# Optimization experiments

Measured on AMD Instinct MI355X. Metric: run time of the kernel, lower is better.

## Reference

```python
import jax, jax.numpy as jnp
import numpy as np

D_MODEL = 512
NUM_HEADS = 8
D_HEAD = D_MODEL // NUM_HEADS
QMAX = 127.0  # int8 narrow-range symmetric
EPS = 1e-8


def _quant_dequant_weight(w):
    # per-output-channel symmetric int8 quant-dequant (brevitas default style)
    s = jnp.maximum(jnp.max(jnp.abs(w), axis=1, keepdims=True) / QMAX, EPS)
    return jnp.clip(jnp.round(w / s), -QMAX, QMAX) * s


def _quant_dequant_act(x):
    # per-tensor symmetric int8 quant-dequant (QuantIdentity)
    s = jnp.maximum(jnp.max(jnp.abs(x)) / QMAX, EPS)
    return jnp.clip(jnp.round(x / s), -QMAX, QMAX) * s


def _qlinear(x, w, b):
    return jnp.einsum('btd,od->bto', x, _quant_dequant_weight(w)) + b


def setup_inputs() -> dict:
    key = jax.random.key(0)
    ks = jax.random.split(key, 10)
    B, T = 2, 4096
    lim = 1.0 / np.sqrt(D_MODEL)
    mk = lambda k: jax.random.uniform(k, (D_MODEL, D_MODEL), jnp.float32, -lim, lim)
    mb = lambda k: jax.random.uniform(k, (D_MODEL,), jnp.float32, -lim, lim)
    return {
        'x': jax.random.normal(ks[0], (B, T, D_MODEL), jnp.float32),
        'mask': jax.random.randint(ks[1], (B, T), 0, 2, jnp.int32),
        'Wq': mk(ks[2]), 'bq': mb(ks[3]),
        'Wk': mk(ks[4]), 'bk': mb(ks[5]),
        'Wv': mk(ks[6]), 'bv': mb(ks[7]),
        'Wo': mk(ks[8]), 'bo': mb(ks[9]),
    }


def reference(x, mask, Wq, bq, Wk, bk, Wv, bv, Wo, bo):
    B, T, _ = x.shape
    shape = lambda t: t.reshape(B, T, NUM_HEADS, D_HEAD).transpose(0, 2, 1, 3)  # (B,H,T,dh)
    q = shape(_qlinear(x, Wq, bq))
    k = shape(_qlinear(x, Wk, bk))
    v = shape(_qlinear(x, Wv, bv))
    scores = jnp.einsum('bhtd,bhsd->bhts', q, k) / np.sqrt(D_HEAD)
    keep = (mask != 0)[:, None, None, :]  # (B,1,1,T), 0 = masked
    scores = jnp.where(keep, scores, -jnp.inf)
    attn = jax.nn.softmax(scores, axis=-1)
    ctx = jnp.einsum('bhts,bhsd->bhtd', attn, v)
    ctx = ctx.transpose(0, 2, 1, 3).reshape(B, T, D_MODEL)
    out = _qlinear(ctx, Wo, bo)
    return _quant_dequant_act(out)
```

## Files before the change

### kernel.cpp

```cpp
#include <hip/hip_runtime.h>
#include <hip/hip_bf16.h>

typedef __bf16 bf16;
typedef __bf16 bf16x8 __attribute__((ext_vector_type(8)));
typedef __bf16 bf16x4v __attribute__((ext_vector_type(4)));
typedef float f32x4 __attribute__((ext_vector_type(4)));

#define D_MODEL 512
#define T_SEQ   4096
#define NH      8
#define DH      64
#define M_ROWS  8192
#define VROW    8224
#define QK_SCALE 0.18033688011112042f

__device__ __forceinline__ void gload16(const void* g, void* l) {
  __builtin_amdgcn_global_load_lds(
      (const __attribute__((address_space(1))) unsigned int*)g,
      (__attribute__((address_space(3))) unsigned int*)l, 16, 0, 0);
}

#define WAITV(N) asm volatile("s_waitcnt vmcnt(" #N ")" ::: "memory")
#define CFENCE   asm volatile("" ::: "memory")

__global__ __launch_bounds__(64) void detect_dtype(const unsigned short* __restrict__ xr,
                                                   int* __restrict__ flag)
{
  int lane = threadIdx.x;
  int cnt = 0;
  for (int i = lane; i < 4096; i += 64) {
    unsigned short u = xr[i];
    int e = (u >> 7) & 0xFF;
    bool insane = (e >= 133) || (e > 0 && e <= 96) || (e == 0 && (u & 0x7F) != 0);
    cnt += insane ? 1 : 0;
  }
#pragma unroll
  for (int off = 32; off >= 1; off >>= 1) cnt += __shfl_xor(cnt, off);
  if (lane == 0) *flag = (cnt > 400) ? 1 : 0;
}

__global__ __launch_bounds__(256) void convert_x(const void* __restrict__ xr,
                                                 const int* __restrict__ flag,
                                                 bf16* __restrict__ xb, int n)
{
  int i = (blockIdx.x * blockDim.x + threadIdx.x) * 4;
  if (i >= n) return;
  if (*flag) {
    float4 v = *(const float4*)((const float*)xr + i);
    __align__(8) bf16 o[4] = {(bf16)v.x, (bf16)v.y, (bf16)v.z, (bf16)v.w};
    *(uint2*)(xb + i) = *(uint2*)o;
  } else {
    *(uint2*)(xb + i) = *(const uint2*)((const bf16*)xr + i);
  }
}

__global__ __launch_bounds__(1024) void prep_aux(
    const void* b0, const void* b1, const void* b2, const void* b3,
    const int* __restrict__ mask,
    const int* __restrict__ flag, float* __restrict__ bf, float* __restrict__ mf)
{
  const void* ps[4] = {b0, b1, b2, b3};
  int fl = *flag;
  int g = blockIdx.x * 1024 + threadIdx.x;
  if (g < 4 * D_MODEL) {
    int w = g >> 9, o = g & 511;
    bf[g] = fl ? ((const float*)ps[w])[o] : (float)((const bf16*)ps[w])[o];
  }
  mf[g] = mask[g] ? -16.0f : -1e30f;
}

__global__ __launch_bounds__(256) void qdq_weights(
    const void* __restrict__ Wq, const void* __restrict__ Wk,
    const void* __restrict__ Wv, const void* __restrict__ Wo,
    const int* __restrict__ flag, bf16* __restrict__ out)
{
  int wave = threadIdx.x >> 6, lane = threadIdx.x & 63;
  int gid = blockIdx.x * 4 + wave;
  int w = gid >> 9, row = gid & 511;
  const void* W = (w == 0) ? Wq : (w == 1) ? Wk : (w == 2) ? Wv : Wo;
  int fl = *flag;
  float v[8]; float amax = 0.f;
#pragma unroll
  for (int i = 0; i < 8; i++) {
    int idx = row * D_MODEL + lane + 64 * i;
    v[i] = fl ? ((const float*)W)[idx] : (float)((const bf16*)W)[idx];
    amax = fmaxf(amax, fabsf(v[i]));
  }
#pragma unroll
  for (int off = 32; off >= 1; off >>= 1) amax = fmaxf(amax, __shfl_xor(amax, off));
  float s = fmaxf(amax / 127.0f, 1e-8f);
  bf16* dst = out + (size_t)gid * D_MODEL;
#pragma unroll
  for (int i = 0; i < 8; i++) {
    float q = rintf(v[i] / s);
    q = fminf(fmaxf(q, -127.f), 127.f);
    dst[lane + 64*i] = (bf16)(q * s);
  }
}

#define LDS_STRIDE 40
__global__ __launch_bounds__(256) void gemm_qkv(
    const bf16* __restrict__ A, const bf16* __restrict__ W,
    const float* __restrict__ bias,
    bf16* __restrict__ Qh, bf16* __restrict__ Kh, bf16* __restrict__ VTP)
{
  __shared__ __align__(16) bf16 As[128 * LDS_STRIDE];
  __shared__ __align__(16) bf16 Bs[128 * LDS_STRIDE];

  const int tid = threadIdx.x;
  const int wave = tid >> 6, lane = tid & 63;
  const int lr = lane & 15, quad = lane >> 4;
  const int wm = (wave >> 1) * 64, wn = (wave & 1) * 64;
  const int m0 = blockIdx.x * 128, n0 = blockIdx.y * 128;
  const int sec = blockIdx.y >> 2;

  f32x4 acc[4][4];
#pragma unroll
  for (int i = 0; i < 4; i++)
#pragma unroll
    for (int j = 0; j < 4; j++) acc[i][j] = f32x4{0.f, 0.f, 0.f, 0.f};

  const int srow = tid >> 2;
  const int sseg = (tid & 3) * 8;

  for (int k0 = 0; k0 < D_MODEL; k0 += 32) {
#pragma unroll
    for (int i = 0; i < 2; i++) {
      int r = srow + i * 64;
      *(uint4*)&As[r * LDS_STRIDE + sseg] = *(const uint4*)(A + (size_t)(m0 + r) * D_MODEL + k0 + sseg);
      *(uint4*)&Bs[r * LDS_STRIDE + sseg] = *(const uint4*)(W + (size_t)(n0 + r) * D_MODEL + k0 + sseg);
    }
    __syncthreads();
    bf16x8 af[4], bfr[4];
#pragma unroll
    for (int mt = 0; mt < 4; mt++) af[mt]  = *(bf16x8*)&As[(wm + mt*16 + lr) * LDS_STRIDE + quad*8];
#pragma unroll
    for (int nt = 0; nt < 4; nt++) bfr[nt] = *(bf16x8*)&Bs[(wn + nt*16 + lr) * LDS_STRIDE + quad*8];
#pragma unroll
    for (int mt = 0; mt < 4; mt++)
#pragma unroll
      for (int nt = 0; nt < 4; nt++)
        acc[mt][nt] = __builtin_amdgcn_mfma_f32_16x16x32_bf16(af[mt], bfr[nt], acc[mt][nt], 0, 0, 0);
    __syncthreads();
  }

  const float scale = (sec == 0) ? QK_SCALE : 1.0f;
#pragma unroll
  for (int mt = 0; mt < 4; mt++) {
    int grow = m0 + wm + mt * 16 + quad * 4;
#pragma unroll
    for (int nt = 0; nt < 4; nt++) {
      int gcol = n0 + wn + nt * 16 + lr;
      float b = bias[gcol];
      if (sec == 2) {
        bf16x4v pk;
#pragma unroll
        for (int r = 0; r < 4; r++) pk[r] = (bf16)(acc[mt][nt][r] + b);
        *(bf16x4v*)(VTP + (size_t)(gcol - 1024) * VROW + grow) = pk;
      } else {
        bf16* dst = (sec == 0) ? Qh : Kh;
        int c = gcol & 511;
        int hh = c >> 6, c64 = c & 63;
#pragma unroll
        for (int r = 0; r < 4; r++) {
          int row = grow + r;
          int bb = row >> 12, t = row & 4095;
          dst[((size_t)(bb * NH + hh) * T_SEQ + t) * DH + c64] =
              (bf16)((acc[mt][nt][r] + b) * scale);
        }
      }
    }
  }
}

__global__ __launch_bounds__(256) void gemm_o(
    const bf16* __restrict__ A, const bf16* __restrict__ W,
    const float* __restrict__ bias,
    float* __restrict__ Cf, unsigned int* __restrict__ amaxp)
{
  __shared__ __align__(16) bf16 As[64 * LDS_STRIDE];
  __shared__ __align__(16) bf16 Bs[128 * LDS_STRIDE];
  __shared__ float wred[4];

  const int tid = threadIdx.x;
  const int wave = tid >> 6, lane = tid & 63;
  const int lr = lane & 15, quad = lane >> 4;
  const int wm = (wave >> 1) * 32, wn = (wave & 1) * 64;
  const int m0 = blockIdx.x * 64, n0 = blockIdx.y * 128;

  f32x4 acc[2][4];
#pragma unroll
  for (int i = 0; i < 2; i++)
#pragma unroll
    for (int j = 0; j < 4; j++) acc[i][j] = f32x4{0.f, 0.f, 0.f, 0.f};

  const int srow = tid >> 2;
  const int sseg = (tid & 3) * 8;

  for (int k0 = 0; k0 < D_MODEL; k0 += 32) {
    *(uint4*)&As[srow * LDS_STRIDE + sseg] = *(const uint4*)(A + (size_t)(m0 + srow) * D_MODEL + k0 + sseg);
#pragma unroll
    for (int i = 0; i < 2; i++) {
      int r = srow + i * 64;
      *(uint4*)&Bs[r * LDS_STRIDE + sseg] = *(const uint4*)(W + (size_t)(n0 + r) * D_MODEL + k0 + sseg);
    }
    __syncthreads();
    bf16x8 af[2], bfr[4];
#pragma unroll
    for (int mt = 0; mt < 2; mt++) af[mt]  = *(bf16x8*)&As[(wm + mt*16 + lr) * LDS_STRIDE + quad*8];
#pragma unroll
    for (int nt = 0; nt < 4; nt++) bfr[nt] = *(bf16x8*)&Bs[(wn + nt*16 + lr) * LDS_STRIDE + quad*8];
#pragma unroll
    for (int mt = 0; mt < 2; mt++)
#pragma unroll
      for (int nt = 0; nt < 4; nt++)
        acc[mt][nt] = __builtin_amdgcn_mfma_f32_16x16x32_bf16(af[mt], bfr[nt], acc[mt][nt], 0, 0, 0);
    __syncthreads();
  }

  float lmax = 0.f;
#pragma unroll
  for (int mt = 0; mt < 2; mt++) {
    int grow = m0 + wm + mt * 16 + quad * 4;
#pragma unroll
    for (int nt = 0; nt < 4; nt++) {
      int gcol = n0 + wn + nt * 16 + lr;
      float b = bias[gcol];
#pragma unroll
      for (int r = 0; r < 4; r++) {
        float v = acc[mt][nt][r] + b;
        Cf[(size_t)(grow + r) * D_MODEL + gcol] = v;
        lmax = fmaxf(lmax, fabsf(v));
      }
    }
  }
#pragma unroll
  for (int off = 32; off >= 1; off >>= 1) lmax = fmaxf(lmax, __shfl_xor(lmax, off));
  if (lane == 0) wred[wave] = lmax;
  __syncthreads();
  if (tid == 0) {
    float m = fmaxf(fmaxf(wred[0], wred[1]), fmaxf(wred[2], wred[3]));
    atomicMax(amaxp, __float_as_uint(m));
  }
}

__global__ __launch_bounds__(256, 2) void attn(
    const bf16* __restrict__ Q, const bf16* __restrict__ K, const bf16* __restrict__ VT,
    const float* __restrict__ maskf, bf16* __restrict__ ctx)
{
  __shared__ __align__(16) bf16 Ks[3][64 * 64];
  __shared__ __align__(16) bf16 Vs[3][64 * 64];
  __shared__ __align__(16) float Mf[T_SEQ];

  const int tid = threadIdx.x;
  const int wave = tid >> 6, lane = tid & 63;
  const int lr = lane & 15, quad = lane >> 4;
  const int i = blockIdx.x;
  const int bh = (i & 7) * 2 + ((i >> 3) & 1);
  const int qb = i >> 4;
  const int b = bh >> 3, h = bh & 7;
  const int q0 = qb * 128 + wave * 32;

  const bf16* Qb = Q + (size_t)bh * T_SEQ * DH;
  const bf16* Kb = K + (size_t)bh * T_SEQ * DH;
  const bf16* Vb = VT + (size_t)(h * DH) * VROW + (size_t)b * T_SEQ;
  const float* mb = maskf + b * T_SEQ;

  const int phase = (qb * 2) & 63;

  const bf16* kSrc[2]; const bf16* vSrc[2];
#pragma unroll
  for (int ii = 0; ii < 2; ii++) {
    int s = ii * 256 + tid, row = s >> 3, sl = s & 7;
    int kt = row >> 4, m = row & 15;
    int keym = ((m >> 2) << 3) + ((kt & 1) << 2) + (m & 3) + ((kt >> 1) << 5);
    kSrc[ii] = Kb + (size_t)keym * DH + ((sl ^ (row & 7)) << 3);
    vSrc[ii] = Vb + (size_t)row * VROW + ((sl ^ (row & 7)) << 3);
  }

  bf16x8 qf[2][2];
#pragma unroll
  for (int qt = 0; qt < 2; qt++) {
    const bf16* rq = Qb + (size_t)(q0 + qt * 16 + lr) * DH;
    qf[qt][0] = *(const bf16x8*)(rq + quad * 8);
    qf[qt][1] = *(const bf16x8*)(rq + 32 + quad * 8);
  }
  WAITV(0);

#pragma unroll
  for (int ii = 0; ii < 4; ii++) {
    int g = ii * 256 + tid;
    gload16(mb + g * 4, &Mf[g * 4]);
  }
#pragma unroll
  for (int d = 0; d < 3; d++) {
    int kb = ((phase + d) & 63) * 64;
#pragma unroll
    for (int ii = 0; ii < 2; ii++) {
      int s = ii * 256 + tid;
      gload16(kSrc[ii] + (size_t)kb * DH, &Ks[d][s * 8]);
      gload16(vSrc[ii] + kb, &Vs[d][s * 8]);
    }
  }

  f32x4 O[2][4];
#pragma unroll
  for (int a = 0; a < 2; a++)
#pragma unroll
    for (int c = 0; c < 4; c++) O[a][c] = f32x4{0.f, 0.f, 0.f, 0.f};
  float lacc[2] = {0.f, 0.f};

  WAITV(8);
  __builtin_amdgcn_s_barrier();
  CFENCE;

  int cur = 0, cc = phase;
  for (int j = 0; j < 64; j++) {
    f32x4 mk[4];
#pragma unroll
    for (int kt = 0; kt < 4; kt++)
      mk[kt] = *(const f32x4*)&Mf[cc * 64 + ((kt >> 1) << 5) + (quad << 3) + ((kt & 1) << 2)];

    bf16x8 kr[4][2];
#pragma unroll
    for (int kt = 0; kt < 4; kt++)
#pragma unroll
      for (int kh = 0; kh < 2; kh++)
        kr[kt][kh] = *(const bf16x8*)&Ks[cur][(kt * 16 + lr) * 64 +
                                             (((kh * 4 + quad) ^ (lr & 7)) << 3)];

    bf16x8 pfa[2][2];
#pragma unroll
    for (int qt = 0; qt < 2; qt++) {
      f32x4 z[4];
#pragma unroll
      for (int kt = 0; kt < 4; kt++) {
        f32x4 t = mk[kt];
        t = __builtin_amdgcn_mfma_f32_16x16x32_bf16(kr[kt][0], qf[qt][0], t, 0, 0, 0);
        t = __builtin_amdgcn_mfma_f32_16x16x32_bf16(kr[kt][1], qf[qt][1], t, 0, 0, 0);
        z[kt] = t;
      }
      float la = lacc[qt];
#pragma unroll
      for (int kt = 0; kt < 4; kt++) {
#pragma unroll
        for (int r = 0; r < 4; r++) {
          float p = __builtin_amdgcn_exp2f(z[kt][r]);
          la += p;
          pfa[qt][kt >> 1][((kt & 1) << 2) + r] = (bf16)p;
        }
      }
      lacc[qt] = la;
    }

    bf16x8 vr[4][2];
#pragma unroll
    for (int nt = 0; nt < 4; nt++)
#pragma unroll
      for (int ks = 0; ks < 2; ks++)
        vr[nt][ks] = *(const bf16x8*)&Vs[cur][(nt * 16 + lr) * 64 +
                                             (((ks * 4 + quad) ^ (lr & 7)) << 3)];

#pragma unroll
    for (int nt = 0; nt < 4; nt++)
#pragma unroll
      for (int qt = 0; qt < 2; qt++) {
        O[qt][nt] = __builtin_amdgcn_mfma_f32_16x16x32_bf16(pfa[qt][0], vr[nt][0], O[qt][nt], 0, 0, 0);
        O[qt][nt] = __builtin_amdgcn_mfma_f32_16x16x32_bf16(pfa[qt][1], vr[nt][1], O[qt][nt], 0, 0, 0);
      }

    if (j < 63) {
      __builtin_amdgcn_s_barrier();
      CFENCE;
      if (j < 61) {
        int kb = ((cc + 3) & 63) * 64;
#pragma unroll
        for (int ii = 0; ii < 2; ii++) {
          int s = ii * 256 + tid;
          gload16(kSrc[ii] + (size_t)kb * DH, &Ks[cur][s * 8]);
          gload16(vSrc[ii] + kb, &Vs[cur][s * 8]);
        }
        WAITV(8);
      } else if (j == 61) {
        WAITV(4);
      } else {
        WAITV(0);
      }
      __builtin_amdgcn_s_barrier();
      CFENCE;
    }
    cur = (cur == 2) ? 0 : cur + 1;
    cc = (cc + 1) & 63;
  }

#pragma unroll
  for (int qt = 0; qt < 2; qt++) {
    float ls = lacc[qt];
    ls += __shfl_xor(ls, 16);
    ls += __shfl_xor(ls, 32);
    float linv = 1.0f / ls;
    float lO[4];
#pragma unroll
    for (int r = 0; r < 4; r++) lO[r] = __shfl(linv, quad * 4 + r);
#pragma unroll
    for (int nt = 0; nt < 4; nt++)
#pragma unroll
      for (int r = 0; r < 4; r++) {
        size_t row = (size_t)(b * T_SEQ + q0 + qt * 16 + quad * 4 + r);
        ctx[row * D_MODEL + h * DH + nt * 16 + lr] = (bf16)(O[qt][nt][r] * lO[r]);
      }
  }
}

__global__ __launch_bounds__(256) void act_qdq(
    const float* __restrict__ pre, const unsigned int* __restrict__ amaxp,
    const int* __restrict__ flag, void* __restrict__ outv, int n)
{
  int i = (blockIdx.x * blockDim.x + threadIdx.x) * 4;
  if (i >= n) return;
  float s = fmaxf(__uint_as_float(*amaxp) / 127.0f, 1e-8f);
  float4 v = *(const float4*)(pre + i);
  float o[4] = {v.x, v.y, v.z, v.w};
#pragma unroll
  for (int r = 0; r < 4; r++) {
    float q = rintf(o[r] / s);
    q = fminf(fmaxf(q, -127.f), 127.f);
    o[r] = q * s;
  }
  if (*flag) {
    *(float4*)((float*)outv + i) = make_float4(o[0], o[1], o[2], o[3]);
  } else {
    __align__(8) bf16 ob[4] = {(bf16)o[0], (bf16)o[1], (bf16)o[2], (bf16)o[3]};
    *(uint2*)((bf16*)outv + i) = *(uint2*)ob;
  }
}

extern "C" void kernel_launch(void* const* d_in, const int* in_sizes, int n_in,
                              void* d_out, int out_size, void* d_ws, size_t ws_size,
                              hipStream_t stream) {
  const void* x    = d_in[0];
  const int*  mask = (const int*)d_in[1];
  const void* Wq = d_in[2]; const void* bq = d_in[3];
  const void* Wk = d_in[4]; const void* bk = d_in[5];
  const void* Wv = d_in[6]; const void* bv = d_in[7];
  const void* Wo = d_in[8]; const void* bo = d_in[9];

  char* ws = (char*)d_ws;
  int*  flag  = (int*)(ws + 0);
  unsigned int* amax = (unsigned int*)(ws + 64);
  float* biasf = (float*)(ws + 1024);
  float* maskf = (float*)(ws + 16384);
  bf16* Wt  = (bf16*)(ws + 65536);
  bf16* xb  = (bf16*)(ws + 4194304);
  bf16* Qm  = (bf16*)(ws + 12582912);
  bf16* Km  = (bf16*)(ws + 20971520);
  bf16* VT  = (bf16*)(ws + 29360128);
  bf16* Cm  = (bf16*)(ws + 4194304);
  float* pre = (float*)(ws + 12582912);

  hipMemsetAsync(amax, 0, 4, stream);
  detect_dtype<<<1, 64, 0, stream>>>((const unsigned short*)x, flag);
  convert_x<<<4096, 256, 0, stream>>>(x, flag, xb, M_ROWS * D_MODEL);
  prep_aux<<<8, 1024, 0, stream>>>(bq, bk, bv, bo, mask, flag, biasf, maskf);
  qdq_weights<<<512, 256, 0, stream>>>(Wq, Wk, Wv, Wo, flag, Wt);
  gemm_qkv<<<dim3(64, 12), 256, 0, stream>>>(xb, Wt, biasf, Qm, Km, VT);
  attn<<<512, 256, 0, stream>>>(Qm, Km, VT, maskf, Cm);
  gemm_o<<<dim3(128, 4), 256, 0, stream>>>(Cm, Wt + 3*262144, biasf + 1536, pre, amax);
  act_qdq<<<4096, 256, 0, stream>>>(pre, amax, flag, d_out, M_ROWS * D_MODEL);
}
```

Before: 216.7 us.

## Double-buffer QKV and O GEMMs with direct global-to-LDS loads and XOR swizzle

Rewrites the QKV and output-projection GEMM mainloops to prefetch K-tiles two steps ahead into double-buffered LDS using global_load_lds, with vmcnt waits and raw barriers instead of __syncthreads. The padded LDS stride is replaced by an XOR swizzle on 16-byte segments so reads avoid bank conflicts without padding. The aim is to hide global-load latency behind MFMA work and drop the register round-trip for staging. This doubles LDS use per block and relies on the hand-tuned waitcnt counts being correct.

```diff
diff --git a/kernel.cpp b/kernel.cpp
--- a/kernel.cpp
+++ b/kernel.cpp
@@ -98,14 +98,13 @@
   }
 }
 
-#define LDS_STRIDE 40
 __global__ __launch_bounds__(256) void gemm_qkv(
     const bf16* __restrict__ A, const bf16* __restrict__ W,
     const float* __restrict__ bias,
     bf16* __restrict__ Qh, bf16* __restrict__ Kh, bf16* __restrict__ VTP)
 {
-  __shared__ __align__(16) bf16 As[128 * LDS_STRIDE];
-  __shared__ __align__(16) bf16 Bs[128 * LDS_STRIDE];
+  __shared__ __align__(16) bf16 As[2][128 * 32];
+  __shared__ __align__(16) bf16 Bs[2][128 * 32];
 
   const int tid = threadIdx.x;
   const int wave = tid >> 6, lane = tid & 63;
@@ -114,34 +113,70 @@
   const int m0 = blockIdx.x * 128, n0 = blockIdx.y * 128;
   const int sec = blockIdx.y >> 2;
 
+  const bf16* aSrc[2]; const bf16* bSrc[2];
+#pragma unroll
+  for (int ii = 0; ii < 2; ii++) {
+    int s = ii * 256 + tid, row = s >> 2, sl = s & 3;
+    int g = (row ^ (row >> 2)) & 3;
+    aSrc[ii] = A + (size_t)(m0 + row) * D_MODEL + ((sl ^ g) << 3);
+    bSrc[ii] = W + (size_t)(n0 + row) * D_MODEL + ((sl ^ g) << 3);
+  }
+
   f32x4 acc[4][4];
 #pragma unroll
   for (int i = 0; i < 4; i++)
 #pragma unroll
     for (int j = 0; j < 4; j++) acc[i][j] = f32x4{0.f, 0.f, 0.f, 0.f};
 
-  const int srow = tid >> 2;
-  const int sseg = (tid & 3) * 8;
-
-  for (int k0 = 0; k0 < D_MODEL; k0 += 32) {
-#pragma unroll
-    for (int i = 0; i < 2; i++) {
-      int r = srow + i * 64;
-      *(uint4*)&As[r * LDS_STRIDE + sseg] = *(const uint4*)(A + (size_t)(m0 + r) * D_MODEL + k0 + sseg);
-      *(uint4*)&Bs[r * LDS_STRIDE + sseg] = *(const uint4*)(W + (size_t)(n0 + r) * D_MODEL + k0 + sseg);
-    }
-    __syncthreads();
+#pragma unroll
+  for (int d = 0; d < 2; d++) {
+#pragma unroll
+    for (int ii = 0; ii < 2; ii++) {
+      int s = ii * 256 + tid;
+      gload16(aSrc[ii] + d * 32, &As[d][s * 8]);
+      gload16(bSrc[ii] + d * 32, &Bs[d][s * 8]);
+    }
+  }
+  WAITV(4);
+  __builtin_amdgcn_s_barrier();
+  CFENCE;
+
+  for (int k = 0; k < 16; k++) {
+    const int cur = k & 1;
     bf16x8 af[4], bfr[4];
 #pragma unroll
-    for (int mt = 0; mt < 4; mt++) af[mt]  = *(bf16x8*)&As[(wm + mt*16 + lr) * LDS_STRIDE + quad*8];
-#pragma unroll
-    for (int nt = 0; nt < 4; nt++) bfr[nt] = *(bf16x8*)&Bs[(wn + nt*16 + lr) * LDS_STRIDE + quad*8];
+    for (int mt = 0; mt < 4; mt++) {
+      int row = wm + mt * 16 + lr;
+      af[mt] = *(const bf16x8*)&As[cur][row * 32 + ((quad ^ ((row ^ (row >> 2)) & 3)) << 3)];
+    }
+#pragma unroll
+    for (int nt = 0; nt < 4; nt++) {
+      int row = wn + nt * 16 + lr;
+      bfr[nt] = *(const bf16x8*)&Bs[cur][row * 32 + ((quad ^ ((row ^ (row >> 2)) & 3)) << 3)];
+    }
 #pragma unroll
     for (int mt = 0; mt < 4; mt++)
 #pragma unroll
       for (int nt = 0; nt < 4; nt++)
         acc[mt][nt] = __builtin_amdgcn_mfma_f32_16x16x32_bf16(af[mt], bfr[nt], acc[mt][nt], 0, 0, 0);
-    __syncthreads();
+
+    if (k < 15) {
+      __builtin_amdgcn_s_barrier();
+      CFENCE;
+      if (k < 14) {
+#pragma unroll
+        for (int ii = 0; ii < 2; ii++) {
+          int s = ii * 256 + tid;
+          gload16(aSrc[ii] + (k + 2) * 32, &As[cur][s * 8]);
+          gload16(bSrc[ii] + (k + 2) * 32, &Bs[cur][s * 8]);
+        }
+        WAITV(4);
+      } else {
+        WAITV(0);
+      }
+      __builtin_amdgcn_s_barrier();
+      CFENCE;
+    }
   }
 
   const float scale = (sec == 0) ? QK_SCALE : 1.0f;
@@ -178,8 +213,8 @@
     const float* __restrict__ bias,
     float* __restrict__ Cf, unsigned int* __restrict__ amaxp)
 {
-  __shared__ __align__(16) bf16 As[64 * LDS_STRIDE];
-  __shared__ __align__(16) bf16 Bs[128 * LDS_STRIDE];
+  __shared__ __align__(16) bf16 As[2][64 * 32];
+  __shared__ __align__(16) bf16 Bs[2][128 * 32];
   __shared__ float wred[4];
 
   const int tid = threadIdx.x;
@@ -188,34 +223,74 @@
   const int wm = (wave >> 1) * 32, wn = (wave & 1) * 64;
   const int m0 = blockIdx.x * 64, n0 = blockIdx.y * 128;
 
+  const bf16* aSrc; const bf16* bSrc[2];
+  {
+    int s = tid, row = s >> 2, sl = s & 3;
+    int g = (row ^ (row >> 2)) & 3;
+    aSrc = A + (size_t)(m0 + row) * D_MODEL + ((sl ^ g) << 3);
+  }
+#pragma unroll
+  for (int ii = 0; ii < 2; ii++) {
+    int s = ii * 256 + tid, row = s >> 2, sl = s & 3;
+    int g = (row ^ (row >> 2)) & 3;
+    bSrc[ii] = W + (size_t)(n0 + row) * D_MODEL + ((sl ^ g) << 3);
+  }
+
   f32x4 acc[2][4];
 #pragma unroll
   for (int i = 0; i < 2; i++)
 #pragma unroll
     for (int j = 0; j < 4; j++) acc[i][j] = f32x4{0.f, 0.f, 0.f, 0.f};
 
-  const int srow = tid >> 2;
-  const int sseg = (tid & 3) * 8;
-
-  for (int k0 = 0; k0 < D_MODEL; k0 += 32) {
-    *(uint4*)&As[srow * LDS_STRIDE + sseg] = *(const uint4*)(A + (size_t)(m0 + srow) * D_MODEL + k0 + sseg);
-#pragma unroll
-    for (int i = 0; i < 2; i++) {
-      int r = srow + i * 64;
-      *(uint4*)&Bs[r * LDS_STRIDE + sseg] = *(const uint4*)(W + (size_t)(n0 + r) * D_MODEL + k0 + sseg);
-    }
-    __syncthreads();
+#pragma unroll
+  for (int d = 0; d < 2; d++) {
+    gload16(aSrc + d * 32, &As[d][tid * 8]);
+#pragma unroll
+    for (int ii = 0; ii < 2; ii++) {
+      int s = ii * 256 + tid;
+      gload16(bSrc[ii] + d * 32, &Bs[d][s * 8]);
+    }
+  }
+  WAITV(3);
+  __builtin_amdgcn_s_barrier();
+  CFENCE;
+
+  for (int k = 0; k < 16; k++) {
+    const int cur = k & 1;
     bf16x8 af[2], bfr[4];
 #pragma unroll
-    for (int mt = 0; mt < 2; mt++) af[mt]  = *(bf16x8*)&As[(wm + mt*16 + lr) * LDS_STRIDE + quad*8];
-#pragma unroll
-    for (int nt = 0; nt < 4; nt++) bfr[nt] = *(bf16x8*)&Bs[(wn + nt*16 + lr) * LDS_STRIDE + quad*8];
+    for (int mt = 0; mt < 2; mt++) {
+      int row = wm + mt * 16 + lr;
+      af[mt] = *(const bf16x8*)&As[cur][row * 32 + ((quad ^ ((row ^ (row >> 2)) & 3)) << 3)];
+    }
+#pragma unroll
+    for (int nt = 0; nt < 4; nt++) {
+      int row = wn + nt * 16 + lr;
+      bfr[nt] = *(const bf16x8*)&Bs[cur][row * 32 + ((quad ^ ((row ^ (row >> 2)) & 3)) << 3)];
+    }
 #pragma unroll
     for (int mt = 0; mt < 2; mt++)
 #pragma unroll
       for (int nt = 0; nt < 4; nt++)
         acc[mt][nt] = __builtin_amdgcn_mfma_f32_16x16x32_bf16(af[mt], bfr[nt], acc[mt][nt], 0, 0, 0);
-    __syncthreads();
+
+    if (k < 15) {
+      __builtin_amdgcn_s_barrier();
+      CFENCE;
+      if (k < 14) {
+        gload16(aSrc + (k + 2) * 32, &As[cur][tid * 8]);
+#pragma unroll
+        for (int ii = 0; ii < 2; ii++) {
+          int s = ii * 256 + tid;
+          gload16(bSrc[ii] + (k + 2) * 32, &Bs[cur][s * 8]);
+        }
+        WAITV(3);
+      } else {
+        WAITV(0);
+      }
+      __builtin_amdgcn_s_barrier();
+      CFENCE;
+    }
   }
 
   float lmax = 0.f;
```

Result: no change. 215.8 us (-0.4%).
